# Performance work log

Measured on AMD Instinct MI355X. Metric: run time of the kernel, lower is better.

The kernel has to match this reference:

```python
import jax, jax.numpy as jnp
import numpy as np

B, C, CI, H, W = 4, 256, 128, 64, 64  # batch, in_channels, inter_channels, spatial


def setup_inputs() -> dict:
    key = jax.random.key(0)
    ks = jax.random.split(key, 9)
    p = lambda k, shape: jax.random.normal(k, shape, jnp.float32) * 0.05
    return {
        "x": jax.random.normal(ks[0], (B, C, H, W), jnp.float32),
        "g_w": p(ks[1], (CI, C)), "g_b": p(ks[2], (CI,)),
        "theta_w": p(ks[3], (CI, C)), "theta_b": p(ks[4], (CI,)),
        "phi_w": p(ks[5], (CI, C)), "phi_b": p(ks[6], (CI,)),
        "out_w": p(ks[7], (C, CI)), "out_b": p(ks[8], (C,)),
    }


def reference(x, g_w, g_b, theta_w, theta_b, phi_w, phi_b, out_w, out_b):
    n, c, h, w = x.shape
    xf = x.reshape(n, c, h * w)  # (b, C, N)
    # 1x1 convs as channel matmuls
    g_x = jnp.einsum('bcn,oc->bno', xf, g_w) + g_b              # (b, N, CI)
    theta_x = jnp.einsum('bcn,oc->bno', xf, theta_w) + theta_b  # (b, N, CI)
    phi_x = jnp.einsum('bcn,oc->bon', xf, phi_w) + phi_b[:, None]  # (b, CI, N)
    # 'channel' whitening: theta centered over channel axis per position,
    # phi centered over spatial axis per channel (as in source)
    theta_x = theta_x - theta_x.mean(axis=2, keepdims=True)
    phi_x = phi_x - phi_x.mean(axis=2, keepdims=True)
    # no softmax / no scaling in this forward
    pairwise = jnp.einsum('bnc,bcm->bnm', theta_x, phi_x)  # (b, N, N)
    y = jnp.einsum('bnm,bmc->bnc', pairwise, g_x)          # (b, N, CI)
    out = jnp.einsum('bnc,oc->bon', y, out_w) + out_b[:, None]  # (b, C, N)
    return x + out.reshape(n, c, h, w)
```

## Files before the change

kernel.cpp:

```cpp
#include <hip/hip_runtime.h>

constexpr int kB  = 4;
constexpr int kC  = 256;
constexpr int kCI = 128;
constexpr int kN  = 64 * 64;


typedef __attribute__((ext_vector_type(8))) short bf16x8;
typedef __attribute__((ext_vector_type(4))) float f32x4;

__device__ inline ushort f2b(float f) {
    unsigned u = __float_as_uint(f);
    return (ushort)((u + 0x7FFF + ((u >> 16) & 1)) >> 16);
}
__device__ inline float b2f(ushort u) { return __uint_as_float((unsigned)u << 16); }

constexpr long kOffTwcT = 0;
constexpr long kOffTbc  = kOffTwcT + kC * kCI;
constexpr long kOffRs   = kOffTbc + kCI;
constexpr long kOffT    = kOffRs + kB * kC;
constexpr long kOffBeta = kOffT + kB * kCI * kCI;
constexpr long kOffPGW  = kOffBeta + kB * kC;
constexpr long kOffMtH  = kOffPGW + (long)kC * kC / 2;
constexpr long kOffXT   = kOffMtH + (long)kB * kC * kC / 2;

__global__ void __launch_bounds__(256, 4)
xt_fused(const float* __restrict__ x, ushort* __restrict__ xT,
         const float* __restrict__ theta_w, const float* __restrict__ theta_b,
         const float* __restrict__ phi_w, const float* __restrict__ g_w,
         float* __restrict__ twcT, float* __restrict__ tbc,
         float* __restrict__ rs, float* __restrict__ T,
         ushort* __restrict__ PGWh) {
    __shared__ __align__(16) float smem[128 * 65];
    int t = threadIdx.x;
    if (blockIdx.y == 4) {
        int idx = blockIdx.z * 64 + blockIdx.x;
        T[(long)idx * 256 + t] = 0.f;
        {
            const float* src = idx < kCI ? phi_w + (long)idx * kC
                                         : g_w + (long)(idx - kCI) * kC;
            if (t < 64) {
                float4 v = *(const float4*)(src + 4 * t);
                ushort4 u = {f2b(v.x), f2b(v.y), f2b(v.z), f2b(v.w)};
                *(ushort4*)(PGWh + (long)idx * kC + 4 * t) = u;
            }
        }
        if (idx >= 4) return;
        __shared__ float part[64][4];
        __shared__ float meanv[64];
        __shared__ float smr[128];
        float (*Ls)[65] = (float(*)[65])smem;
        int blk = idx, c0 = blk * 64;
        rs[blk * 256 + t] = 0.f;
#pragma unroll
        for (int it = 0; it < 8; it++) {
            int l = t + 256 * it;
            int k = l >> 4, c4 = (l & 15) * 4;
            float4 v = *(const float4*)(theta_w + (long)k * kC + c0 + c4);
            Ls[k][c4 + 0] = v.x; Ls[k][c4 + 1] = v.y;
            Ls[k][c4 + 2] = v.z; Ls[k][c4 + 3] = v.w;
        }
        __syncthreads();
        {
            int c = t >> 2, q = t & 3;
            float s = 0.f;
#pragma unroll
            for (int k = 0; k < 32; k++) s += Ls[q * 32 + k][c];
            part[c][q] = s;
        }
        __syncthreads();
        if (t < 64)
            meanv[t] = (part[t][0] + part[t][1] + part[t][2] + part[t][3]) * (1.f / kCI);
        __syncthreads();
        {
            int c = t >> 2, ks = (t & 3) * 32;
            float* dst = twcT + (long)(c0 + c) * kCI + ks;
            float m = meanv[c];
#pragma unroll
            for (int k = 0; k < 32; k++) dst[k] = Ls[ks + k][c] - m;
        }
        if (blk == 0) {
            if (t < 128) smr[t] = theta_b[t];
            __syncthreads();
            for (int st = 64; st > 0; st >>= 1) {
                if (t < st) smr[t] += smr[t + st];
                __syncthreads();
            }
            float bmean = smr[0] * (1.f / kCI);
            if (t < 128) tbc[t] = theta_b[t] - bmean;
        }
        return;
    }
    int b = blockIdx.z;
    int n0 = blockIdx.x * 64, c0 = blockIdx.y * 64;
    float (*ft)[66] = (float(*)[66])smem;
    const float* xb = x + (long)b * kC * kN;
#pragma unroll
    for (int i = 0; i < 4; i++) {
        int l = t + 256 * i;
        int row = l >> 4, col4 = (l & 15) * 4;
        float4 v = *(const float4*)(xb + (long)(c0 + row) * kN + n0 + col4);
        ft[row][col4 + 0] = v.x; ft[row][col4 + 1] = v.y;
        ft[row][col4 + 2] = v.z; ft[row][col4 + 3] = v.w;
    }
    __syncthreads();
    {
        int n = t >> 2, cs = (t & 3) * 16;
        unsigned w[8];
#pragma unroll
        for (int j = 0; j < 8; j++) {
            ushort lo = f2b(ft[cs + 2 * j][n]);
            ushort hi = f2b(ft[cs + 2 * j + 1][n]);
            w[j] = (unsigned)lo | ((unsigned)hi << 16);
        }
        ushort* dst = xT + ((long)b * kN + n0 + n) * kC + c0 + cs;
        ((uint4*)dst)[0] = make_uint4(w[0], w[1], w[2], w[3]);
        ((uint4*)dst)[1] = make_uint4(w[4], w[5], w[6], w[7]);
    }
}

__global__ void __launch_bounds__(256, 2)
pgt_mfma(const ushort* __restrict__ PGWh, const ushort* __restrict__ xT,
         float* __restrict__ rs, float* __restrict__ T) {
    int b = blockIdx.z;
    int n0 = blockIdx.x * 64;
    __shared__ ushort Ws[256 * 40];
    __shared__ ushort Xs[64 * 40];
    __shared__ ushort PGs[256 * 72];
    int t = threadIdx.x;
    int w = t >> 6, lane = t & 63, q = lane >> 4, ln = lane & 15;
    f32x4 acc[4][4];
#pragma unroll
    for (int i = 0; i < 4; i++)
#pragma unroll
        for (int j = 0; j < 4; j++) acc[i][j] = 0.f;
    const ushort* xTb = xT + ((long)b * kN + n0) * kC;
    for (int kc = 0; kc < kC; kc += 32) {
        __syncthreads();
#pragma unroll
        for (int it = 0; it < 4; it++) {
            int l = t + 256 * it;
            int row = l >> 2, seg = l & 3;
            *(uint4*)&Ws[row * 40 + seg * 8] =
                *(const uint4*)(PGWh + (long)row * kC + kc + seg * 8);
        }
        {
            int row = t >> 2, seg = t & 3;
            *(uint4*)&Xs[row * 40 + seg * 8] =
                *(const uint4*)(xTb + (long)row * kC + kc + seg * 8);
        }
        __syncthreads();
        bf16x8 a[4], bb[4];
#pragma unroll
        for (int mt = 0; mt < 4; mt++)
            a[mt] = *(const bf16x8*)&Ws[(64 * w + 16 * mt + ln) * 40 + q * 8];
#pragma unroll
        for (int nt = 0; nt < 4; nt++)
            bb[nt] = *(const bf16x8*)&Xs[(16 * nt + ln) * 40 + q * 8];
#pragma unroll
        for (int mt = 0; mt < 4; mt++)
#pragma unroll
            for (int nt = 0; nt < 4; nt++)
                acc[mt][nt] = __builtin_amdgcn_mfma_f32_16x16x32_bf16(
                    a[mt], bb[nt], acc[mt][nt], 0, 0, 0);
    }
    float rpart[4][4] = {};
#pragma unroll
    for (int mt = 0; mt < 4; mt++)
#pragma unroll
        for (int nt = 0; nt < 4; nt++)
#pragma unroll
            for (int i = 0; i < 4; i++) {
                int row = 64 * w + 16 * mt + 4 * q + i;
                int col = 16 * nt + ln;
                ushort st = f2b(acc[mt][nt][i]);
                PGs[row * 72 + col] = st;
                rpart[mt][i] += b2f(st);
            }
#pragma unroll
    for (int mt = 0; mt < 4; mt++)
#pragma unroll
        for (int i = 0; i < 4; i++) {
            float v = rpart[mt][i];
            v += __shfl_xor(v, 1);
            v += __shfl_xor(v, 2);
            v += __shfl_xor(v, 4);
            v += __shfl_xor(v, 8);
            if (ln == 0)
                atomicAdd(rs + b * kC + 64 * w + 16 * mt + 4 * q + i, v);
        }
    __syncthreads();
    f32x4 acc2[2][8];
#pragma unroll
    for (int i = 0; i < 2; i++)
#pragma unroll
        for (int j = 0; j < 8; j++) acc2[i][j] = 0.f;
#pragma unroll
    for (int kk = 0; kk < 64; kk += 32) {
        bf16x8 a2[2], b2[8];
#pragma unroll
        for (int mt = 0; mt < 2; mt++)
            a2[mt] = *(const bf16x8*)&PGs[(32 * w + 16 * mt + ln) * 72 + kk + q * 8];
#pragma unroll
        for (int nt = 0; nt < 8; nt++)
            b2[nt] = *(const bf16x8*)&PGs[(128 + 16 * nt + ln) * 72 + kk + q * 8];
#pragma unroll
        for (int mt = 0; mt < 2; mt++)
#pragma unroll
            for (int nt = 0; nt < 8; nt++)
                acc2[mt][nt] = __builtin_amdgcn_mfma_f32_16x16x32_bf16(
                    a2[mt], b2[nt], acc2[mt][nt], 0, 0, 0);
    }
    float* Tb = T + (long)b * kCI * kCI;
#pragma unroll
    for (int mt = 0; mt < 2; mt++)
#pragma unroll
        for (int nt = 0; nt < 8; nt++)
#pragma unroll
            for (int i = 0; i < 4; i++) {
                int c  = 32 * w + 16 * mt + 4 * q + i;
                int cp = 16 * nt + ln;
                atomicAdd(&Tb[(long)c * kCI + cp], acc2[mt][nt][i]);
            }
}

__global__ void __launch_bounds__(256, 2)
wm_kernel(const float* __restrict__ out_w, const float* __restrict__ T,
          const float* __restrict__ rs, const float* __restrict__ twcT,
          const float* __restrict__ tbc, const float* __restrict__ out_b,
          ushort* __restrict__ Mth, float* __restrict__ beta) {
    int b = blockIdx.z;
    int m0 = blockIdx.y * 64, n0 = blockIdx.x * 64;
    const float* Tb = T + (long)b * kCI * kCI;
    __shared__ __align__(16) float As[16][68];
    __shared__ __align__(16) float Bs[16][132];
    __shared__ __align__(16) float W2s[128][68];
    int t = threadIdx.x;
    int tr = t >> 4, tc = t & 15;
    float accA[4][8] = {};
    for (int c0 = 0; c0 < kCI; c0 += 16) {
        __syncthreads();
        {
            int r = t >> 2, c4 = (t & 3) * 4;
            float4 va = *(const float4*)(out_w + (long)(m0 + r) * kCI + c0 + c4);
            As[c4 + 0][r] = va.x; As[c4 + 1][r] = va.y;
            As[c4 + 2][r] = va.z; As[c4 + 3][r] = va.w;
        }
#pragma unroll
        for (int it = 0; it < 2; it++) {
            int l = t + 256 * it;
            int r = l >> 2, c4 = (l & 3) * 4;
            float4 vb = *(const float4*)(Tb + (long)r * kCI + c0 + c4);
            float rp = rs[b * kC + r] * (1.f / kN);
            const float* rg = rs + b * kC + kCI + c0 + c4;
            vb.x -= rp * rg[0]; vb.y -= rp * rg[1];
            vb.z -= rp * rg[2]; vb.w -= rp * rg[3];
            Bs[c4 + 0][r] = vb.x; Bs[c4 + 1][r] = vb.y;
            Bs[c4 + 2][r] = vb.z; Bs[c4 + 3][r] = vb.w;
        }
        __syncthreads();
#pragma unroll
        for (int k = 0; k < 16; k++) {
            float4 a = *(const float4*)&As[k][4 * tr];
            float4 b0 = *(const float4*)&Bs[k][8 * tc];
            float4 b1 = *(const float4*)&Bs[k][8 * tc + 4];
            float av[4] = {a.x, a.y, a.z, a.w};
            float bw[8] = {b0.x, b0.y, b0.z, b0.w, b1.x, b1.y, b1.z, b1.w};
#pragma unroll
            for (int i = 0; i < 4; i++)
#pragma unroll
                for (int j = 0; j < 8; j++) accA[i][j] += av[i] * bw[j];
        }
    }
    __syncthreads();
#pragma unroll
    for (int i = 0; i < 4; i++)
#pragma unroll
        for (int j = 0; j < 8; j++) W2s[8 * tc + j][4 * tr + i] = accA[i][j];
    __syncthreads();
    if (blockIdx.x == 0 && t < 64) {
        float s = out_b[m0 + t];
#pragma unroll 8
        for (int j = 0; j < kCI; j++) s += tbc[j] * W2s[j][t];
        beta[b * kC + m0 + t] = s;
    }
    int ty = t >> 4, tx = t & 15;
    float accB[4][4] = {};
    for (int j0 = 0; j0 < kCI; j0 += 16) {
        __syncthreads();
        {
            int r = t >> 2, c4 = (t & 3) * 4;
            float4 vb = *(const float4*)(twcT + (long)(n0 + r) * kCI + j0 + c4);
            As[c4 + 0][r] = vb.x; As[c4 + 1][r] = vb.y;
            As[c4 + 2][r] = vb.z; As[c4 + 3][r] = vb.w;
        }
        __syncthreads();
#pragma unroll
        for (int k = 0; k < 16; k++) {
            float4 a = *(const float4*)&W2s[j0 + k][4 * ty];
            float4 bv = *(const float4*)&As[k][4 * tx];
            float av[4] = {a.x, a.y, a.z, a.w};
            float bw[4] = {bv.x, bv.y, bv.z, bv.w};
#pragma unroll
            for (int i = 0; i < 4; i++)
#pragma unroll
                for (int j = 0; j < 4; j++) accB[i][j] += av[i] * bw[j];
        }
    }
    ushort* Cb = Mth + (long)b * kC * kC;
#pragma unroll
    for (int i = 0; i < 4; i++) {
        ushort4 u = {f2b(accB[i][0]), f2b(accB[i][1]), f2b(accB[i][2]), f2b(accB[i][3])};
        *(ushort4*)(Cb + (long)(m0 + 4 * ty + i) * kC + n0 + 4 * tx) = u;
    }
}

__global__ void __launch_bounds__(256, 2)
final_mfma(const float* __restrict__ x, const ushort* __restrict__ Mth,
           const ushort* __restrict__ xT, const float* __restrict__ beta,
           float* __restrict__ out) {
    int b = blockIdx.z;
    int o0 = blockIdx.y * 128, n0 = blockIdx.x * 128;
    const ushort* Mbh = Mth + (long)b * kC * kC;
    __shared__ ushort Ws[128 * 40];
    __shared__ ushort Xs[128 * 40];
    int t = threadIdx.x;
    int w = t >> 6, lane = t & 63, q = lane >> 4, ln = lane & 15;
    f32x4 acc[2][8];
#pragma unroll
    for (int i = 0; i < 2; i++)
#pragma unroll
        for (int j = 0; j < 8; j++) acc[i][j] = 0.f;
    const ushort* xTb = xT + ((long)b * kN + n0) * kC;
    for (int kc = 0; kc < kC; kc += 32) {
        __syncthreads();
#pragma unroll
        for (int it = 0; it < 2; it++) {
            int l = t + 256 * it;
            int row = l >> 2, seg = l & 3;
            uint4 v = *(const uint4*)(Mbh + (long)(o0 + row) * kC + kc + seg * 8);
            *(uint4*)&Ws[row * 40 + seg * 8] = v;
        }
#pragma unroll
        for (int it = 0; it < 2; it++) {
            int l = t + 256 * it;
            int row = l >> 2, seg = l & 3;
            uint4 v = *(const uint4*)(xTb + (long)row * kC + kc + seg * 8);
            *(uint4*)&Xs[row * 40 + seg * 8] = v;
        }
        __syncthreads();
        bf16x8 a[2], bb[8];
#pragma unroll
        for (int mt = 0; mt < 2; mt++)
            a[mt] = *(const bf16x8*)&Ws[(32 * w + 16 * mt + ln) * 40 + q * 8];
#pragma unroll
        for (int nt = 0; nt < 8; nt++)
            bb[nt] = *(const bf16x8*)&Xs[(16 * nt + ln) * 40 + q * 8];
#pragma unroll
        for (int mt = 0; mt < 2; mt++)
#pragma unroll
            for (int nt = 0; nt < 8; nt++)
                acc[mt][nt] = __builtin_amdgcn_mfma_f32_16x16x32_bf16(
                    a[mt], bb[nt], acc[mt][nt], 0, 0, 0);
    }
    const float* xb = x + (long)b * kC * kN;
    float* ob = out + (long)b * kC * kN;
#pragma unroll
    for (int mt = 0; mt < 2; mt++)
#pragma unroll
        for (int nt = 0; nt < 8; nt++)
#pragma unroll
            for (int i = 0; i < 4; i++) {
                int row = o0 + 32 * w + 16 * mt + 4 * q + i;
                int col = n0 + 16 * nt + ln;
                long idx = (long)row * kN + col;
                ob[idx] = acc[mt][nt][i] + xb[idx] + beta[b * kC + row];
            }
}

extern "C" void kernel_launch(void* const* d_in, const int* in_sizes, int n_in,
                              void* d_out, int out_size, void* d_ws, size_t ws_size,
                              hipStream_t stream) {
    const float* x       = (const float*)d_in[0];
    const float* g_w     = (const float*)d_in[1];
    const float* theta_w = (const float*)d_in[3];
    const float* theta_b = (const float*)d_in[4];
    const float* phi_w   = (const float*)d_in[5];
    const float* out_w   = (const float*)d_in[7];
    const float* out_b   = (const float*)d_in[8];
    float* out = (float*)d_out;
    float* ws  = (float*)d_ws;

    float*  twcT = ws + kOffTwcT;
    float*  tbc  = ws + kOffTbc;
    float*  rs   = ws + kOffRs;
    float*  T    = ws + kOffT;
    float*  beta = ws + kOffBeta;
    ushort* PGWh = (ushort*)(ws + kOffPGW);
    ushort* Mth  = (ushort*)(ws + kOffMtH);
    ushort* xT   = (ushort*)(ws + kOffXT);

    xt_fused<<<dim3(kN / 64, 5, kB), 256, 0, stream>>>(
        x, xT, theta_w, theta_b, phi_w, g_w, twcT, tbc, rs, T, PGWh);
    pgt_mfma<<<dim3(kN / 64, 1, kB), 256, 0, stream>>>(PGWh, xT, rs, T);
    wm_kernel<<<dim3(4, 4, kB), 256, 0, stream>>>(out_w, T, rs, twcT, tbc,
                                                  out_b, Mth, beta);
    final_mfma<<<dim3(kN / 128, 2, kB), 256, 0, stream>>>(x, Mth, xT, beta, out);
}
```

Measured before the change: 150.4 us.

## Split fused PG/T kernel into materialized PG pass and split-K T reduction

The combined kernel that computed phi/g projections and immediately accumulated the per-tile T=phi·gᵀ product with heavy fp32 atomics is split in two. The first kernel writes the bf16 PG projections to a global workspace using larger 128x128 tiles. The second computes T with a 16-way split over the spatial axis, which cuts the number of atomic adds into T. This trades many atomics per 64-column tile for an extra global write and read of a B*256*N bf16 buffer and one more launch.

```diff
diff --git a/kernel.cpp b/kernel.cpp
--- a/kernel.cpp
+++ b/kernel.cpp
@@ -5,6 +5,9 @@
 constexpr int kCI = 128;
 constexpr int kN  = 64 * 64;
 
+
+constexpr int kSplits = 16;
+constexpr int kSliceN = kN / kSplits;
 
 typedef __attribute__((ext_vector_type(8))) short bf16x8;
 typedef __attribute__((ext_vector_type(4))) float f32x4;
@@ -21,7 +24,8 @@
 constexpr long kOffT    = kOffRs + kB * kC;
 constexpr long kOffBeta = kOffT + kB * kCI * kCI;
 constexpr long kOffPGW  = kOffBeta + kB * kC;
-constexpr long kOffMtH  = kOffPGW + (long)kC * kC / 2;
+constexpr long kOffPG   = kOffPGW + (long)kC * kC / 2;
+constexpr long kOffMtH  = kOffPG + (long)kB * kC * kN / 2;
 constexpr long kOffXT   = kOffMtH + (long)kB * kC * kC / 2;
 
 __global__ void __launch_bounds__(256, 4)
@@ -120,65 +124,68 @@
 }
 
 __global__ void __launch_bounds__(256, 2)
-pgt_mfma(const ushort* __restrict__ PGWh, const ushort* __restrict__ xT,
-         float* __restrict__ rs, float* __restrict__ T) {
+pg_mfma(const ushort* __restrict__ PGWh, const ushort* __restrict__ xT,
+        ushort* __restrict__ PGh, float* __restrict__ rs) {
     int b = blockIdx.z;
-    int n0 = blockIdx.x * 64;
-    __shared__ ushort Ws[256 * 40];
-    __shared__ ushort Xs[64 * 40];
-    __shared__ ushort PGs[256 * 72];
+    int r0 = blockIdx.y * 128, n0 = blockIdx.x * 128;
+    __shared__ ushort Ws[128 * 40];
+    __shared__ ushort Xs[128 * 40];
     int t = threadIdx.x;
     int w = t >> 6, lane = t & 63, q = lane >> 4, ln = lane & 15;
-    f32x4 acc[4][4];
-#pragma unroll
-    for (int i = 0; i < 4; i++)
-#pragma unroll
-        for (int j = 0; j < 4; j++) acc[i][j] = 0.f;
+    f32x4 acc[2][8];
+#pragma unroll
+    for (int i = 0; i < 2; i++)
+#pragma unroll
+        for (int j = 0; j < 8; j++) acc[i][j] = 0.f;
     const ushort* xTb = xT + ((long)b * kN + n0) * kC;
+    const ushort* Wb  = PGWh + (long)r0 * kC;
     for (int kc = 0; kc < kC; kc += 32) {
         __syncthreads();
 #pragma unroll
-        for (int it = 0; it < 4; it++) {
+        for (int it = 0; it < 2; it++) {
             int l = t + 256 * it;
             int row = l >> 2, seg = l & 3;
             *(uint4*)&Ws[row * 40 + seg * 8] =
-                *(const uint4*)(PGWh + (long)row * kC + kc + seg * 8);
-        }
-        {
-            int row = t >> 2, seg = t & 3;
+                *(const uint4*)(Wb + (long)row * kC + kc + seg * 8);
+        }
+#pragma unroll
+        for (int it = 0; it < 2; it++) {
+            int l = t + 256 * it;
+            int row = l >> 2, seg = l & 3;
             *(uint4*)&Xs[row * 40 + seg * 8] =
                 *(const uint4*)(xTb + (long)row * kC + kc + seg * 8);
         }
         __syncthreads();
-        bf16x8 a[4], bb[4];
-#pragma unroll
-        for (int mt = 0; mt < 4; mt++)
-            a[mt] = *(const bf16x8*)&Ws[(64 * w + 16 * mt + ln) * 40 + q * 8];
-#pragma unroll
-        for (int nt = 0; nt < 4; nt++)
+        bf16x8 a[2], bb[8];
+#pragma unroll
+        for (int mt = 0; mt < 2; mt++)
+            a[mt] = *(const bf16x8*)&Ws[(32 * w + 16 * mt + ln) * 40 + q * 8];
+#pragma unroll
+        for (int nt = 0; nt < 8; nt++)
             bb[nt] = *(const bf16x8*)&Xs[(16 * nt + ln) * 40 + q * 8];
 #pragma unroll
-        for (int mt = 0; mt < 4; mt++)
-#pragma unroll
-            for (int nt = 0; nt < 4; nt++)
+        for (int mt = 0; mt < 2; mt++)
+#pragma unroll
+            for (int nt = 0; nt < 8; nt++)
                 acc[mt][nt] = __builtin_amdgcn_mfma_f32_16x16x32_bf16(
                     a[mt], bb[nt], acc[mt][nt], 0, 0, 0);
     }
-    float rpart[4][4] = {};
-#pragma unroll
-    for (int mt = 0; mt < 4; mt++)
-#pragma unroll
-        for (int nt = 0; nt < 4; nt++)
+    ushort* pb = PGh + (long)b * kC * kN;
+    float rpart[2][4] = {};
+#pragma unroll
+    for (int mt = 0; mt < 2; mt++)
+#pragma unroll
+        for (int nt = 0; nt < 8; nt++)
 #pragma unroll
             for (int i = 0; i < 4; i++) {
-                int row = 64 * w + 16 * mt + 4 * q + i;
-                int col = 16 * nt + ln;
+                int row = r0 + 32 * w + 16 * mt + 4 * q + i;
+                int col = n0 + 16 * nt + ln;
                 ushort st = f2b(acc[mt][nt][i]);
-                PGs[row * 72 + col] = st;
+                pb[(long)row * kN + col] = st;
                 rpart[mt][i] += b2f(st);
             }
 #pragma unroll
-    for (int mt = 0; mt < 4; mt++)
+    for (int mt = 0; mt < 2; mt++)
 #pragma unroll
         for (int i = 0; i < 4; i++) {
             float v = rpart[mt][i];
@@ -187,41 +194,50 @@
             v += __shfl_xor(v, 4);
             v += __shfl_xor(v, 8);
             if (ln == 0)
-                atomicAdd(rs + b * kC + 64 * w + 16 * mt + 4 * q + i, v);
-        }
-    __syncthreads();
-    f32x4 acc2[2][8];
-#pragma unroll
-    for (int i = 0; i < 2; i++)
-#pragma unroll
-        for (int j = 0; j < 8; j++) acc2[i][j] = 0.f;
-#pragma unroll
-    for (int kk = 0; kk < 64; kk += 32) {
-        bf16x8 a2[2], b2[8];
-#pragma unroll
-        for (int mt = 0; mt < 2; mt++)
-            a2[mt] = *(const bf16x8*)&PGs[(32 * w + 16 * mt + ln) * 72 + kk + q * 8];
-#pragma unroll
-        for (int nt = 0; nt < 8; nt++)
-            b2[nt] = *(const bf16x8*)&PGs[(128 + 16 * nt + ln) * 72 + kk + q * 8];
-#pragma unroll
-        for (int mt = 0; mt < 2; mt++)
-#pragma unroll
-            for (int nt = 0; nt < 8; nt++)
-                acc2[mt][nt] = __builtin_amdgcn_mfma_f32_16x16x32_bf16(
-                    a2[mt], b2[nt], acc2[mt][nt], 0, 0, 0);
+                atomicAdd(rs + b * kC + r0 + 32 * w + 16 * mt + 4 * q + i, v);
+        }
+}
+
+__global__ void __launch_bounds__(256, 4)
+tsplit_mfma(const ushort* __restrict__ PGh, float* __restrict__ T) {
+    int s = blockIdx.x, b = blockIdx.z;
+    int qy = blockIdx.y >> 1, qx = blockIdx.y & 1;
+    long nbase = (long)s * kSliceN;
+    __shared__ ushort As[64 * 40];
+    __shared__ ushort Bs[64 * 40];
+    int t = threadIdx.x;
+    int w = t >> 6, lane = t & 63, q = lane >> 4, ln = lane & 15;
+    f32x4 acc[4];
+#pragma unroll
+    for (int j = 0; j < 4; j++) acc[j] = 0.f;
+    const ushort* Phi = PGh + ((long)b * kC + 64 * qy) * kN + nbase;
+    const ushort* G2  = PGh + ((long)b * kC + kCI + 64 * qx) * kN + nbase;
+    for (int kc = 0; kc < kSliceN; kc += 32) {
+        __syncthreads();
+        {
+            int row = t >> 2, seg = t & 3;
+            *(uint4*)&As[row * 40 + seg * 8] =
+                *(const uint4*)(Phi + (long)row * kN + kc + seg * 8);
+            *(uint4*)&Bs[row * 40 + seg * 8] =
+                *(const uint4*)(G2 + (long)row * kN + kc + seg * 8);
+        }
+        __syncthreads();
+        bf16x8 a = *(const bf16x8*)&As[(16 * w + ln) * 40 + q * 8];
+#pragma unroll
+        for (int nt = 0; nt < 4; nt++) {
+            bf16x8 bb = *(const bf16x8*)&Bs[(16 * nt + ln) * 40 + q * 8];
+            acc[nt] = __builtin_amdgcn_mfma_f32_16x16x32_bf16(a, bb, acc[nt], 0, 0, 0);
+        }
     }
     float* Tb = T + (long)b * kCI * kCI;
 #pragma unroll
-    for (int mt = 0; mt < 2; mt++)
-#pragma unroll
-        for (int nt = 0; nt < 8; nt++)
-#pragma unroll
-            for (int i = 0; i < 4; i++) {
-                int c  = 32 * w + 16 * mt + 4 * q + i;
-                int cp = 16 * nt + ln;
-                atomicAdd(&Tb[(long)c * kCI + cp], acc2[mt][nt][i]);
-            }
+    for (int nt = 0; nt < 4; nt++)
+#pragma unroll
+        for (int i = 0; i < 4; i++) {
+            int c  = 64 * qy + 16 * w + 4 * q + i;
+            int cp = 64 * qx + 16 * nt + ln;
+            atomicAdd(&Tb[(long)c * kCI + cp], acc[nt][i]);
+        }
 }
 
 __global__ void __launch_bounds__(256, 2)
@@ -397,12 +413,14 @@
     float*  T    = ws + kOffT;
     float*  beta = ws + kOffBeta;
     ushort* PGWh = (ushort*)(ws + kOffPGW);
+    ushort* PGh  = (ushort*)(ws + kOffPG);
     ushort* Mth  = (ushort*)(ws + kOffMtH);
     ushort* xT   = (ushort*)(ws + kOffXT);
 
     xt_fused<<<dim3(kN / 64, 5, kB), 256, 0, stream>>>(
         x, xT, theta_w, theta_b, phi_w, g_w, twcT, tbc, rs, T, PGWh);
-    pgt_mfma<<<dim3(kN / 64, 1, kB), 256, 0, stream>>>(PGWh, xT, rs, T);
+    pg_mfma<<<dim3(kN / 128, 2, kB), 256, 0, stream>>>(PGWh, xT, PGh, rs);
+    tsplit_mfma<<<dim3(kSplits, 4, kB), 256, 0, stream>>>(PGh, T);
     wm_kernel<<<dim3(4, 4, kB), 256, 0, stream>>>(out_w, T, rs, twcT, tbc,
                                                   out_b, Mth, beta);
     final_mfma<<<dim3(kN / 128, 2, kB), 256, 0, stream>>>(x, Mth, xT, beta, out);
```

Measured after the change: 139.1 us, median of 2. 7.5% less time.
